# Optimization experiments

Hardware: AMD Instinct MI355X
Metric: run time of the kernel (lower is better)

## Reference

```python
import jax, jax.numpy as jnp
import numpy as np

V, D, H, L, F, S_MAX = 30522, 768, 12, 12, 3072, 512
B, S = 4, 512
HD = D // H
EPS = 1e-5

def setup_inputs():
    key = jax.random.key(0)
    ks = jax.random.split(key, 16)
    s = 0.02
    inp = {
        'input_ids': jax.random.randint(ks[0], (B, S), 0, V),
        'attention_mask': jnp.ones((B, S), dtype=jnp.int32),
        'word_emb': jax.random.normal(ks[1], (V, D)) * s,
        'pos_emb': jax.random.normal(ks[2], (S_MAX, D)) * s,
        'seg_emb': jax.random.normal(ks[3], (2, D)) * s,
        'emb_ln_g': jnp.ones((D,)), 'emb_ln_b': jnp.zeros((D,)),
        # per-layer stacked params, leading dim L
        'Wq': jax.random.normal(ks[4], (L, D, D)) * s,
        'Wk': jax.random.normal(ks[5], (L, D, D)) * s,
        'Wv': jax.random.normal(ks[6], (L, D, D)) * s,
        'Wo': jax.random.normal(ks[7], (L, D, D)) * s,
        'ff1_w': jax.random.normal(ks[8], (L, D, F)) * s,
        'ff1_b': jnp.zeros((L, F)),
        'ff2_w': jax.random.normal(ks[9], (L, F, D)) * s,
        'ff2_b': jnp.zeros((L, D)),
        'ln1_g': jnp.ones((L, D)), 'ln1_b': jnp.zeros((L, D)),
        'ln2_g': jnp.ones((L, D)), 'ln2_b': jnp.zeros((L, D)),
        'out_w': jax.random.normal(ks[10], (D, V)) * s,
        'out_b': jnp.zeros((V,)),
    }
    return inp

def _ln(x, g, b):
    mu = jnp.mean(x, axis=-1, keepdims=True)
    var = jnp.mean(jnp.square(x - mu), axis=-1, keepdims=True)
    return (x - mu) * jax.lax.rsqrt(var + EPS) * g + b

def reference(input_ids, attention_mask, word_emb, pos_emb, seg_emb,
              emb_ln_g, emb_ln_b, Wq, Wk, Wv, Wo, ff1_w, ff1_b, ff2_w, ff2_b,
              ln1_g, ln1_b, ln2_g, ln2_b, out_w, out_b):
    b, s = input_ids.shape
    # embeddings: word + position + segment (segment ids are all zero buffer)
    emb = word_emb[input_ids] + pos_emb[:s][None, :, :] + seg_emb[0][None, None, :]
    x = _ln(emb, emb_ln_g, emb_ln_b)  # [B,S,D]
    # key-position mask: True where masked out. [B,1,1,S]
    neg_mask = (attention_mask == 0)[:, None, None, :]
    scale = 1.0 / jnp.sqrt(jnp.asarray(D, x.dtype))  # NOTE: embed_dim, not head_dim

    def layer(x, p):
        wq, wk, wv, wo, f1w, f1b, f2w, f2b, g1, b1, g2, b2 = p
        q = (x @ wq).reshape(b, s, H, HD)
        k = (x @ wk).reshape(b, s, H, HD)
        v = (x @ wv).reshape(b, s, H, HD)
        scores = jnp.einsum('bqhd,bkhd->bhqk', q, k) * scale  # [B,H,S,S]
        scores = jnp.where(neg_mask, -jnp.inf, scores)
        attn = jax.nn.softmax(scores, axis=-1)
        o = jnp.einsum('bhqk,bkhd->bqhd', attn, v).reshape(b, s, D) @ wo
        x1 = _ln(x + o, g1, b1)
        h = jax.nn.gelu(x1 @ f1w + f1b, approximate=False)  # torch GELU is exact erf
        x2 = _ln(x1 + h @ f2w + f2b, g2, b2)
        return x2, attn

    x, attn_scores = jax.lax.scan(
        layer, x,
        (Wq, Wk, Wv, Wo, ff1_w, ff1_b, ff2_w, ff2_b, ln1_g, ln1_b, ln2_g, ln2_b))
    logits = x @ out_w + out_b  # [B,S,V]
    return logits, attn_scores  # attn_scores: [L,B,H,S,S]
```

## Files before the change

### kernel.cpp

```cpp
#include <hip/hip_runtime.h>
#include <hip/hip_bf16.h>

#define NLAYER 12
#define DMODEL 768
#define NHEAD  12
#define HDIM   64
#define FDIM   3072
#define VOCAB  30522
#define SLEN   512
#define NBATCH 4
#define NTOK   (NBATCH*SLEN)
#define EPSLN  1e-5f

typedef unsigned short u16;
using bf16 = __hip_bfloat16;
typedef __bf16 bf16x8 __attribute__((ext_vector_type(8)));
typedef float  f32x4  __attribute__((ext_vector_type(4)));
typedef u16    u16x4  __attribute__((ext_vector_type(4)));

__device__ __forceinline__ u16 f2bs(float f) {
    bf16 h = __float2bfloat16(f);
    return *reinterpret_cast<u16*>(&h);
}

__device__ __forceinline__ void gload_lds16(const void* g, void* l) {
    auto gp = (const __attribute__((address_space(1))) unsigned int*)g;
    auto lp = (__attribute__((address_space(3))) unsigned int*)(unsigned long long)l;
    __builtin_amdgcn_global_load_lds(gp, lp, 16, 0, 0);
}

template<int N> __device__ __forceinline__ void waitv() {
    if constexpr (N == 0)      asm volatile("s_waitcnt vmcnt(0)" ::: "memory");
    else if constexpr (N == 3) asm volatile("s_waitcnt vmcnt(3)" ::: "memory");
    else if constexpr (N == 4) asm volatile("s_waitcnt vmcnt(4)" ::: "memory");
    else if constexpr (N == 6) asm volatile("s_waitcnt vmcnt(6)" ::: "memory");
    else if constexpr (N == 8) asm volatile("s_waitcnt vmcnt(8)" ::: "memory");
}

__device__ __forceinline__ float wave_sum64(float v) {
#pragma unroll
    for (int off = 32; off > 0; off >>= 1) v += __shfl_down(v, off, 64);
    return v;
}
__device__ __forceinline__ float block_sum256(float v, float* red) {
    v = wave_sum64(v);
    __syncthreads();
    if ((threadIdx.x & 63) == 0) red[threadIdx.x >> 6] = v;
    __syncthreads();
    return red[0] + red[1] + red[2] + red[3];
}

__global__ __launch_bounds__(256) void embed_ln_kernel(
    const int* __restrict__ ids, const float* __restrict__ word,
    const float* __restrict__ pos, const float* __restrict__ seg,
    const float* __restrict__ g, const float* __restrict__ b,
    float* __restrict__ out, u16* __restrict__ outb)
{
    __shared__ float red[4];
    int t = blockIdx.x;
    int s = t & (SLEN - 1);
    long woff = (long)ids[t] * DMODEL;
    float vals[3];
#pragma unroll
    for (int i = 0; i < 3; i++) {
        int d = threadIdx.x + i * 256;
        vals[i] = word[woff + d] + pos[(long)s * DMODEL + d] + seg[d];
    }
    float mu = block_sum256(vals[0] + vals[1] + vals[2], red) * (1.0f / DMODEL);
    float vv = 0.f;
#pragma unroll
    for (int i = 0; i < 3; i++) { float d0 = vals[i] - mu; vv += d0 * d0; }
    float rstd = rsqrtf(block_sum256(vv, red) * (1.0f / DMODEL) + EPSLN);
#pragma unroll
    for (int i = 0; i < 3; i++) {
        int d = threadIdx.x + i * 256;
        float r = (vals[i] - mu) * rstd * g[d] + b[d];
        out[(long)t * DMODEL + d] = r;
        outb[(long)t * DMODEL + d] = f2bs(r);
    }
}

__global__ __launch_bounds__(256) void ln_res2_kernel(
    const float* __restrict__ a, const float* __restrict__ p0,
    const float* __restrict__ p1, const float* __restrict__ cbias,
    const float* __restrict__ g, const float* __restrict__ beta,
    float* __restrict__ out, u16* __restrict__ outb)
{
    __shared__ float red[4];
    long t = blockIdx.x;
    float vals[3];
#pragma unroll
    for (int i = 0; i < 3; i++) {
        int d = threadIdx.x + i * 256;
        float bb = cbias ? cbias[d] : 0.f;
        vals[i] = a[t * DMODEL + d] + p0[t * DMODEL + d] + p1[t * DMODEL + d] + bb;
    }
    float mu = block_sum256(vals[0] + vals[1] + vals[2], red) * (1.0f / DMODEL);
    float vv = 0.f;
#pragma unroll
    for (int i = 0; i < 3; i++) { float d0 = vals[i] - mu; vv += d0 * d0; }
    float rstd = rsqrtf(block_sum256(vv, red) * (1.0f / DMODEL) + EPSLN);
#pragma unroll
    for (int i = 0; i < 3; i++) {
        int d = threadIdx.x + i * 256;
        float r = (vals[i] - mu) * rstd * g[d] + beta[d];
        out[t * DMODEL + d] = r;
        outb[t * DMODEL + d] = f2bs(r);
    }
}

__global__ __launch_bounds__(256) void ln_res4_kernel(
    const float* __restrict__ a, const float* __restrict__ p0,
    const float* __restrict__ p1, const float* __restrict__ p2,
    const float* __restrict__ p3, const float* __restrict__ cbias,
    const float* __restrict__ g, const float* __restrict__ beta,
    float* __restrict__ out, u16* __restrict__ outb)
{
    __shared__ float red[4];
    long t = blockIdx.x;
    float vals[3];
#pragma unroll
    for (int i = 0; i < 3; i++) {
        int d = threadIdx.x + i * 256;
        vals[i] = a[t * DMODEL + d] + p0[t * DMODEL + d] + p1[t * DMODEL + d]
                + p2[t * DMODEL + d] + p3[t * DMODEL + d] + cbias[d];
    }
    float mu = block_sum256(vals[0] + vals[1] + vals[2], red) * (1.0f / DMODEL);
    float vv = 0.f;
#pragma unroll
    for (int i = 0; i < 3; i++) { float d0 = vals[i] - mu; vv += d0 * d0; }
    float rstd = rsqrtf(block_sum256(vv, red) * (1.0f / DMODEL) + EPSLN);
#pragma unroll
    for (int i = 0; i < 3; i++) {
        int d = threadIdx.x + i * 256;
        float r = (vals[i] - mu) * rstd * g[d] + beta[d];
        out[t * DMODEL + d] = r;
        outb[t * DMODEL + d] = f2bs(r);
    }
}

#define DD (DMODEL*DMODEL)
#define DF (DMODEL*FDIM)
#define LAYER_W_ELEMS (4*DD + 2*DF)
#define TILES_DD 576
#define TILES_DF 2304
#define TILES_LAYER (4*TILES_DD + 2*TILES_DF)
#define TILES_ALL (NLAYER*TILES_LAYER)
#define NTX_OW ((VOCAB + 31) / 32)
#define TILES_OW (NTX_OW * (DMODEL/32))

__global__ __launch_bounds__(256) void conv_all_kernel(
    const float* __restrict__ Wq, const float* __restrict__ Wk,
    const float* __restrict__ Wv, const float* __restrict__ Wo,
    const float* __restrict__ F1w, const float* __restrict__ F2w,
    const float* __restrict__ OutW, u16* __restrict__ wT, u16* __restrict__ owT)
{
    __shared__ float t[32][33];
    int id = blockIdx.x;
    const float* src; u16* dst; int K, N, tt;
    if (id < TILES_ALL) {
        int l = id / TILES_LAYER, r = id - l * TILES_LAYER;
        u16* base = wT + (long)l * LAYER_W_ELEMS;
        if (r < TILES_DD)           { src = Wq  + (long)l * DD; dst = base;            K = DMODEL; N = DMODEL; tt = r; }
        else if (r < 2 * TILES_DD)  { src = Wk  + (long)l * DD; dst = base + DD;       K = DMODEL; N = DMODEL; tt = r - TILES_DD; }
        else if (r < 3 * TILES_DD)  { src = Wv  + (long)l * DD; dst = base + 2 * DD;   K = DMODEL; N = DMODEL; tt = r - 2 * TILES_DD; }
        else if (r < 4 * TILES_DD)  { src = Wo  + (long)l * DD; dst = base + 3 * DD;   K = DMODEL; N = DMODEL; tt = r - 3 * TILES_DD; }
        else if (r < 4 * TILES_DD + TILES_DF)
                                    { src = F1w + (long)l * DF; dst = base + 4 * DD;   K = DMODEL; N = FDIM;   tt = r - 4 * TILES_DD; }
        else                        { src = F2w + (long)l * DF; dst = base + 4 * DD + DF; K = FDIM; N = DMODEL; tt = r - 4 * TILES_DD - TILES_DF; }
    } else {
        src = OutW; dst = owT; K = DMODEL; N = VOCAB; tt = id - TILES_ALL;
    }
    int ntx = (N + 31) >> 5;
    int n0 = (tt % ntx) * 32, k0 = (tt / ntx) * 32;
    int tx = threadIdx.x & 31, ty = threadIdx.x >> 5;
#pragma unroll
    for (int i = 0; i < 32; i += 8) {
        int k = k0 + ty + i, n = n0 + tx;
        t[ty + i][tx] = (k < K && n < N) ? src[(long)k * N + n] : 0.f;
    }
    __syncthreads();
#pragma unroll
    for (int i = 0; i < 32; i += 8) {
        int n = n0 + ty + i, k = k0 + tx;
        if (n < N && k < K) dst[(long)n * K + k] = f2bs(t[tx][ty + i]);
    }
}

__global__ __launch_bounds__(256, 2) void attn_kernel(
    const u16* __restrict__ qkvb, const u16* __restrict__ vtb,
    const int* __restrict__ amask,
    float* __restrict__ attn, u16* __restrict__ ob)
{
    __shared__ u16 Qs[64][64];
    __shared__ u16 Ks[SLEN][64];
    __shared__ float maskadd[SLEN];
    __shared__ __align__(16) float redA[64][4];
    __shared__ __align__(16) float redB[64][4];

    u16* Ph = &Ks[0][0];
    u16* Vh = &Ks[256][0];

    int z = blockIdx.y;
    int b = z / NHEAD, h = z - b * NHEAD;
    int m0 = blockIdx.x * 64;
    int tid = threadIdx.x;
    int wave = tid >> 6, lane = tid & 63;
    int quad = lane >> 4, l16 = lane & 15;
    const float scale = 0.036084391824351615f;

    for (int i = tid; i < SLEN; i += 256)
        maskadd[i] = amask[b * SLEN + i] ? 0.f : -1e30f;

    const u16* Qbase = qkvb + (long)(b * SLEN) * (3 * DMODEL) + h * HDIM;
    const u16* Kbase = Qbase + DMODEL;
    const u16* Vtbase = vtb + (long)z * HDIM * SLEN;

#pragma unroll
    for (int i = 0; i < 2; i++) {
        int off = wave * 2048 + i * 1024 + lane * 16;
        int row = off >> 7, c = (off >> 4) & 7, g = c ^ (row & 7);
        gload_lds16(Qbase + (long)(m0 + row) * (3 * DMODEL) + g * 8,
                    (char*)&Qs[0][0] + wave * 2048 + i * 1024);
    }
#pragma unroll
    for (int i = 0; i < 16; i++) {
        int off = wave * 16384 + i * 1024 + lane * 16;
        int row = off >> 7, c = (off >> 4) & 7, g = c ^ (row & 7);
        gload_lds16(Kbase + (long)row * (3 * DMODEL) + g * 8,
                    (char*)&Ks[0][0] + wave * 16384 + i * 1024);
    }
    __syncthreads();

    f32x4 acc[4][8];
#pragma unroll
    for (int i = 0; i < 4; i++)
#pragma unroll
        for (int j = 0; j < 8; j++) acc[i][j] = (f32x4){0.f, 0.f, 0.f, 0.f};

#pragma unroll
    for (int ks = 0; ks < 2; ks++) {
        bf16x8 afr[4], bfr[8];
#pragma unroll
        for (int i = 0; i < 4; i++) {
            int row = i * 16 + l16;
            int slot = ((ks << 2) + quad) ^ (row & 7);
            afr[i] = *reinterpret_cast<const bf16x8*>((char*)&Qs[0][0] + row * 128 + slot * 16);
        }
#pragma unroll
        for (int j = 0; j < 8; j++) {
            int row = wave * 128 + j * 16 + l16;
            int slot = ((ks << 2) + quad) ^ (row & 7);
            bfr[j] = *reinterpret_cast<const bf16x8*>((char*)&Ks[0][0] + row * 128 + slot * 16);
        }
#pragma unroll
        for (int i = 0; i < 4; i++)
#pragma unroll
            for (int j = 0; j < 8; j++)
                acc[i][j] = __builtin_amdgcn_mfma_f32_16x16x32_bf16(afr[i], bfr[j], acc[i][j], 0, 0, 0);
    }

    float ma[8];
#pragma unroll
    for (int j = 0; j < 8; j++) ma[j] = maskadd[wave * 128 + j * 16 + l16];

    float rmax[4][4];
#pragma unroll
    for (int i = 0; i < 4; i++)
#pragma unroll
        for (int r = 0; r < 4; r++) {
            float m = -3e38f;
#pragma unroll
            for (int j = 0; j < 8; j++) m = fmaxf(m, acc[i][j][r] * scale + ma[j]);
            rmax[i][r] = m;
        }
#pragma unroll
    for (int off = 1; off < 16; off <<= 1)
#pragma unroll
        for (int i = 0; i < 4; i++)
#pragma unroll
            for (int r = 0; r < 4; r++)
                rmax[i][r] = fmaxf(rmax[i][r], __shfl_xor(rmax[i][r], off, 64));
    if (l16 == 0) {
#pragma unroll
        for (int i = 0; i < 4; i++)
#pragma unroll
            for (int r = 0; r < 4; r++) redA[i * 16 + quad * 4 + r][wave] = rmax[i][r];
    }
    __syncthreads();

    {
        const u16* Vb = Vtbase + 0;
#pragma unroll
        for (int i = 0; i < 8; i++) {
            int o = wave * 8192 + i * 1024 + lane * 16;
            int hd = o >> 9, c = (o >> 4) & 31, g = c ^ (hd & 7);
            gload_lds16(Vb + (long)hd * SLEN + g * 8, (char*)Vh + wave * 8192 + i * 1024);
        }
    }

#pragma unroll
    for (int i = 0; i < 4; i++)
#pragma unroll
        for (int r = 0; r < 4; r++) {
            f32x4 v = *reinterpret_cast<const f32x4*>(&redA[i * 16 + quad * 4 + r][0]);
            rmax[i][r] = fmaxf(fmaxf(v[0], v[1]), fmaxf(v[2], v[3]));
        }

    float rsum[4][4];
#pragma unroll
    for (int i = 0; i < 4; i++)
#pragma unroll
        for (int r = 0; r < 4; r++) {
            float s = 0.f;
#pragma unroll
            for (int j = 0; j < 8; j++) {
                float e = expf(acc[i][j][r] * scale + ma[j] - rmax[i][r]);
                acc[i][j][r] = e;
                s += e;
            }
            rsum[i][r] = s;
        }
#pragma unroll
    for (int off = 1; off < 16; off <<= 1)
#pragma unroll
        for (int i = 0; i < 4; i++)
#pragma unroll
            for (int r = 0; r < 4; r++)
                rsum[i][r] += __shfl_xor(rsum[i][r], off, 64);
    if (l16 == 0) {
#pragma unroll
        for (int i = 0; i < 4; i++)
#pragma unroll
            for (int r = 0; r < 4; r++) redB[i * 16 + quad * 4 + r][wave] = rsum[i][r];
    }
    __syncthreads();

    float* ap = attn + (long)z * SLEN * SLEN;
#pragma unroll
    for (int i = 0; i < 4; i++)
#pragma unroll
        for (int r = 0; r < 4; r++) {
            f32x4 v = *reinterpret_cast<const f32x4*>(&redB[i * 16 + quad * 4 + r][0]);
            float inv = 1.0f / (v[0] + v[1] + v[2] + v[3]);
            long row = m0 + i * 16 + quad * 4 + r;
#pragma unroll
            for (int j = 0; j < 8; j++) {
                int col = (wave << 7) + j * 16 + l16;
                float p = acc[i][j][r] * inv;
                acc[i][j][r] = p;
                ap[row * SLEN + col] = p;
            }
        }

    if (wave < 2) {
#pragma unroll
        for (int i = 0; i < 4; i++)
#pragma unroll
            for (int j = 0; j < 8; j++) {
                int cl = (wave << 7) + j * 16 + l16;
#pragma unroll
                for (int r = 0; r < 4; r++) {
                    int row = i * 16 + quad * 4 + r;
                    int slot = (cl >> 3) ^ (row & 7);
                    *(u16*)((char*)Ph + row * 512 + slot * 16 + (cl & 7) * 2) = f2bs(acc[i][j][r]);
                }
            }
    }
    __syncthreads();

    f32x4 acc2[4];
#pragma unroll
    for (int j = 0; j < 4; j++) acc2[j] = (f32x4){0.f, 0.f, 0.f, 0.f};

#pragma unroll
    for (int step = 0; step < 8; step++) {
        int Prow = (wave << 4) + l16;
        int aslot = (step * 4 + quad) ^ (Prow & 7);
        bf16x8 af = *reinterpret_cast<const bf16x8*>((char*)Ph + Prow * 512 + aslot * 16);
#pragma unroll
        for (int j = 0; j < 4; j++) {
            int hd = j * 16 + l16;
            int bslot = (step * 4 + quad) ^ (hd & 7);
            bf16x8 bf = *reinterpret_cast<const bf16x8*>((char*)Vh + hd * 512 + bslot * 16);
            acc2[j] = __builtin_amdgcn_mfma_f32_16x16x32_bf16(af, bf, acc2[j], 0, 0, 0);
        }
    }
    __syncthreads();

    {
        const u16* Vb = Vtbase + 256;
#pragma unroll
        for (int i = 0; i < 8; i++) {
            int o = wave * 8192 + i * 1024 + lane * 16;
            int hd = o >> 9, c = (o >> 4) & 31, g = c ^ (hd & 7);
            gload_lds16(Vb + (long)hd * SLEN + g * 8, (char*)Vh + wave * 8192 + i * 1024);
        }
    }
    if (wave >= 2) {
#pragma unroll
        for (int i = 0; i < 4; i++)
#pragma unroll
            for (int j = 0; j < 8; j++) {
                int cl = ((wave - 2) << 7) + j * 16 + l16;
#pragma unroll
                for (int r = 0; r < 4; r++) {
                    int row = i * 16 + quad * 4 + r;
                    int slot = (cl >> 3) ^ (row & 7);
                    *(u16*)((char*)Ph + row * 512 + slot * 16 + (cl & 7) * 2) = f2bs(acc[i][j][r]);
                }
            }
    }
    __syncthreads();

#pragma unroll
    for (int step = 0; step < 8; step++) {
        int Prow = (wave << 4) + l16;
        int aslot = (step * 4 + quad) ^ (Prow & 7);
        bf16x8 af = *reinterpret_cast<const bf16x8*>((char*)Ph + Prow * 512 + aslot * 16);
#pragma unroll
        for (int j = 0; j < 4; j++) {
            int hd = j * 16 + l16;
            int bslot = (step * 4 + quad) ^ (hd & 7);
            bf16x8 bf = *reinterpret_cast<const bf16x8*>((char*)Vh + hd * 512 + bslot * 16);
            acc2[j] = __builtin_amdgcn_mfma_f32_16x16x32_bf16(af, bf, acc2[j], 0, 0, 0);
        }
    }

#pragma unroll
    for (int j = 0; j < 4; j++)
#pragma unroll
        for (int r = 0; r < 4; r++) {
            int q = m0 + (wave << 4) + quad * 4 + r;
            ob[((long)(b * SLEN + q)) * DMODEL + h * HDIM + j * 16 + l16] = f2bs(acc2[j][r]);
        }
}

template<int BM, int BN, int OUTBF, int GELU, int QKVF>
__global__ __launch_bounds__(256) void gemm_bf16(
    const u16* __restrict__ A, int lda, long sA1, long sA2,
    const u16* __restrict__ B, int ldb, long sB1, long sB2,
    void* __restrict__ Cv, int ldc, long sC1, long sC2,
    int zdiv, const float* __restrict__ bias,
    int N, int K, float scale, u16* __restrict__ vt)
{
    __shared__ u16 As[3][BM][32];
    __shared__ u16 Bs[3][BN][32];
    int z = blockIdx.z;
    int zq = z / zdiv, zr = z - zq * zdiv;
    A += zq * sA1 + zr * sA2;
    B += zq * sB1 + zr * sB2;

    int m0 = blockIdx.y * BM;
    int n0 = blockIdx.x * BN;
    int tid = threadIdx.x;
    int wave = tid >> 6, lane = tid & 63;
    int quad = lane >> 4, l16 = lane & 15;
    int wr = wave >> 1, wc = wave & 1;
    constexpr int MR = BM / 32, NR = BN / 32;
    constexpr int LPT = BM / 64 + BN / 64;

    f32x4 acc[MR][NR];
#pragma unroll
    for (int i = 0; i < MR; i++)
#pragma unroll
        for (int j = 0; j < NR; j++) acc[i][j] = (f32x4){0.f, 0.f, 0.f, 0.f};

    int srow = lane >> 2;
    int sc   = lane & 3;

    auto stage = [&](int buf, int k0) {
#pragma unroll
        for (int i = 0; i < BM / 64; i++) {
            int chunk = wave * (BM / 64) + i;
            int lrow = chunk * 16 + srow;
            int gcol = (sc ^ ((lrow >> 1) & 3)) * 8;
            gload_lds16(A + (long)(m0 + lrow) * lda + k0 + gcol, &As[buf][chunk * 16][0]);
        }
#pragma unroll
        for (int i = 0; i < BN / 64; i++) {
            int chunk = wave * (BN / 64) + i;
            int lrow = chunk * 16 + srow;
            int grow = n0 + lrow;
            if (grow > N - 1) grow = N - 1;
            int gcol = (sc ^ ((lrow >> 1) & 3)) * 8;
            gload_lds16(B + (long)grow * ldb + k0 + gcol, &Bs[buf][chunk * 16][0]);
        }
    };

    int nt = K >> 5;
    stage(0, 0);
    if (nt > 1) stage(1, 32);
    if (nt > 2) stage(2, 64);

    int cur = 0;
    for (int t = 0; t < nt; ++t) {
        if (t + 2 < nt)      waitv<2 * LPT>();
        else if (t + 1 < nt) waitv<LPT>();
        else                 waitv<0>();
        __builtin_amdgcn_s_barrier();
        __builtin_amdgcn_sched_barrier(0);

        bf16x8 afr[MR], bfr[NR];
#pragma unroll
        for (int i = 0; i < MR; i++) {
            int row = wr * (BM / 2) + i * 16 + l16;
            int slot = quad ^ ((row >> 1) & 3);
            afr[i] = *reinterpret_cast<const bf16x8*>((char*)&As[cur][0][0] + row * 64 + slot * 16);
        }
#pragma unroll
        for (int j = 0; j < NR; j++) {
            int row = wc * (BN / 2) + j * 16 + l16;
            int slot = quad ^ ((row >> 1) & 3);
            bfr[j] = *reinterpret_cast<const bf16x8*>((char*)&Bs[cur][0][0] + row * 64 + slot * 16);
        }
        __builtin_amdgcn_s_setprio(1);
#pragma unroll
        for (int i = 0; i < MR; i++)
#pragma unroll
            for (int j = 0; j < NR; j++)
                acc[i][j] = __builtin_amdgcn_mfma_f32_16x16x32_bf16(afr[i], bfr[j], acc[i][j], 0, 0, 0);
        __builtin_amdgcn_s_setprio(0);

        asm volatile("" ::: "memory");
        __builtin_amdgcn_sched_barrier(0);
        __builtin_amdgcn_s_barrier();
        __builtin_amdgcn_sched_barrier(0);
        if (t + 3 < nt) stage(cur, (t + 3) * 32);
        cur = cur + 1; if (cur == 3) cur = 0;
    }

    float* Cf = (float*)Cv;
    u16*   Cb = (u16*)Cv;
    long coff = zq * sC1 + zr * sC2;
#pragma unroll
    for (int i = 0; i < MR; i++) {
        int rbase = m0 + wr * (BM / 2) + i * 16 + quad * 4;
#pragma unroll
        for (int j = 0; j < NR; j++) {
            int col = n0 + wc * (BN / 2) + j * 16 + l16;
            if (col < N) {
                float badd = bias ? bias[col] : 0.f;
                u16x4 v4;
#pragma unroll
                for (int r = 0; r < 4; r++) {
                    float vv = acc[i][j][r] * scale + badd;
                    if (GELU) vv = 0.5f * vv * (1.0f + erff(vv * 0.70710678118f));
                    long idx = coff + (long)(rbase + r) * ldc + col;
                    if (OUTBF) { u16 u = f2bs(vv); Cb[idx] = u; v4[r] = u; }
                    else       Cf[idx] = vv;
                }
                if (QKVF && col >= 2 * DMODEL) {
                    int hh = (col - 2 * DMODEL) >> 6, hd = col & 63;
                    int bb = rbase >> 9, s = rbase & (SLEN - 1);
                    *reinterpret_cast<u16x4*>(
                        vt + ((long)(bb * NHEAD + hh) * HDIM + hd) * SLEN + s) = v4;
                }
            }
        }
    }
}

template<int BM, int BN, int OUTBF, int GELU, int QKVF = 0>
static inline void launch_gemm(hipStream_t stream,
    const u16* A, int lda, long sA1, long sA2,
    const u16* B, int ldb, long sB1, long sB2,
    void* C, int ldc, long sC1, long sC2,
    int zdiv, const float* bias, int M, int N, int K, float scale, int Z,
    u16* vt = nullptr)
{
    dim3 grid((N + BN - 1) / BN, M / BM, Z);
    gemm_bf16<BM, BN, OUTBF, GELU, QKVF><<<grid, 256, 0, stream>>>(
        A, lda, sA1, sA2, B, ldb, sB1, sB2, C, ldc, sC1, sC2,
        zdiv, bias, N, K, scale, vt);
}

extern "C" void kernel_launch(void* const* d_in, const int* in_sizes, int n_in,
                              void* d_out, int out_size, void* d_ws, size_t ws_size,
                              hipStream_t stream)
{
    const int*   ids   = (const int*)d_in[0];
    const int*   amask = (const int*)d_in[1];
    const float* word  = (const float*)d_in[2];
    const float* pos   = (const float*)d_in[3];
    const float* seg   = (const float*)d_in[4];
    const float* eg    = (const float*)d_in[5];
    const float* eb    = (const float*)d_in[6];
    const float* Wq    = (const float*)d_in[7];
    const float* Wk    = (const float*)d_in[8];
    const float* Wv    = (const float*)d_in[9];
    const float* Wo    = (const float*)d_in[10];
    const float* F1w   = (const float*)d_in[11];
    const float* F1b   = (const float*)d_in[12];
    const float* F2w   = (const float*)d_in[13];
    const float* F2b   = (const float*)d_in[14];
    const float* G1    = (const float*)d_in[15];
    const float* B1    = (const float*)d_in[16];
    const float* G2    = (const float*)d_in[17];
    const float* B2    = (const float*)d_in[18];
    const float* OutW  = (const float*)d_in[19];
    const float* OutB  = (const float*)d_in[20];

    float* logits = (float*)d_out;
    float* attn_base = logits + (long)NTOK * VOCAB;

    long nd = (long)NTOK * DMODEL;
    float* x  = (float*)d_ws;
    float* x1 = x + nd;
    float* p0 = x1 + nd;
    float* p1 = p0 + nd;
    float* p2 = p1 + nd;
    float* p3 = p2 + nd;
    u16* xb   = (u16*)(p3 + nd);
    u16* x1b  = xb + nd;
    u16* qkvb = x1b + nd;
    u16* vtb  = qkvb + (long)NTOK * 3 * DMODEL;
    u16* ob   = vtb + nd;
    u16* hb   = ob + nd;
    u16* wT   = hb + (long)NTOK * FDIM;
    u16* owT  = wT + (long)NLAYER * LAYER_W_ELEMS;

    conv_all_kernel<<<TILES_ALL + TILES_OW, 256, 0, stream>>>(
        Wq, Wk, Wv, Wo, F1w, F2w, OutW, wT, owT);

    embed_ln_kernel<<<NTOK, 256, 0, stream>>>(ids, word, pos, seg, eg, eb, x, xb);

    for (int l = 0; l < NLAYER; l++) {
        const u16* qkvT = wT + (long)l * LAYER_W_ELEMS;
        const u16* woT  = qkvT + 3 * DD;
        const u16* f1T  = qkvT + 4 * DD;
        const u16* f2T  = qkvT + 4 * DD + DF;
        const float* f1b = F1b + (long)l * FDIM;
        const float* f2b = F2b + (long)l * DMODEL;
        float* attn_l = attn_base + (long)l * NBATCH * NHEAD * SLEN * SLEN;

        launch_gemm<128, 128, 1, 0, 1>(stream, xb, DMODEL, 0, 0,
                                       qkvT, DMODEL, 0, 0,
                                       qkvb, 3 * DMODEL, 0, 0,
                                       1, nullptr, NTOK, 3 * DMODEL, DMODEL, 1.f, 1, vtb);

        attn_kernel<<<dim3(SLEN / 64, NBATCH * NHEAD), 256, 0, stream>>>(
            qkvb, vtb, amask, attn_l, ob);

        launch_gemm<128, 64, 0, 0>(stream, ob, DMODEL, 384, 0,
                                   woT, DMODEL, 384, 0,
                                   p0, DMODEL, nd, 0,
                                   1, nullptr, NTOK, DMODEL, 384, 1.f, 2);

        ln_res2_kernel<<<NTOK, 256, 0, stream>>>(x, p0, p1, nullptr,
                                                 G1 + (long)l * DMODEL, B1 + (long)l * DMODEL, x1, x1b);

        launch_gemm<128, 128, 1, 1>(stream, x1b, DMODEL, 0, 0,
                                    f1T, DMODEL, 0, 0,
                                    hb, FDIM, 0, 0,
                                    1, f1b, NTOK, FDIM, DMODEL, 1.f, 1);

        launch_gemm<128, 128, 0, 0>(stream, hb, FDIM, 768, 0,
                                    f2T, FDIM, 768, 0,
                                    p0, DMODEL, nd, 0,
                                    1, nullptr, NTOK, DMODEL, 768, 1.f, 4);

        ln_res4_kernel<<<NTOK, 256, 0, stream>>>(x1, p0, p1, p2, p3, f2b,
                                                 G2 + (long)l * DMODEL, B2 + (long)l * DMODEL, x, xb);
    }

    launch_gemm<128, 128, 0, 0>(stream, xb, DMODEL, 0, 0,
                                owT, DMODEL, 0, 0,
                                logits, VOCAB, 0, 0,
                                1, OutB, NTOK, VOCAB, DMODEL, 1.f, 1);
}
```

Before: 1.907 ms.

## Restructure GEMM to 512 threads, K-tile 64 with double buffering

The bf16 GEMM moves from 256 to 512 threads per block, laid out as a 2x4 wave grid, so each wave now covers half as many N columns. The K tile grows from 32 to 64 with a new XOR swizzle over 8 slots, and the pipeline drops from triple to double buffering. The aim is fewer barriers per unit of K and more waves to hide latency. In exchange each wave does less work per barrier and keeps only one prefetch stage in flight, and the stage code assumes BM and BN are multiples of 64.

Result: faster. 1.758 ms (-7.8%).

```diff
diff --git a/kernel.cpp b/kernel.cpp
--- a/kernel.cpp
+++ b/kernel.cpp
@@ -437,15 +437,15 @@
 }
 
 template<int BM, int BN, int OUTBF, int GELU, int QKVF>
-__global__ __launch_bounds__(256) void gemm_bf16(
+__global__ __launch_bounds__(512) void gemm_bf16(
     const u16* __restrict__ A, int lda, long sA1, long sA2,
     const u16* __restrict__ B, int ldb, long sB1, long sB2,
     void* __restrict__ Cv, int ldc, long sC1, long sC2,
     int zdiv, const float* __restrict__ bias,
     int N, int K, float scale, u16* __restrict__ vt)
 {
-    __shared__ u16 As[3][BM][32];
-    __shared__ u16 Bs[3][BN][32];
+    __shared__ u16 As[2][BM][64];
+    __shared__ u16 Bs[2][BN][64];
     int z = blockIdx.z;
     int zq = z / zdiv, zr = z - zq * zdiv;
     A += zq * sA1 + zr * sA2;
@@ -456,9 +456,10 @@
     int tid = threadIdx.x;
     int wave = tid >> 6, lane = tid & 63;
     int quad = lane >> 4, l16 = lane & 15;
-    int wr = wave >> 1, wc = wave & 1;
-    constexpr int MR = BM / 32, NR = BN / 32;
-    constexpr int LPT = BM / 64 + BN / 64;
+    int wr = wave >> 2, wc = wave & 3;
+    constexpr int MR = BM / 32, NR = BN / 64;
+    constexpr int PA = BM / 64, PB = BN / 64;
+    constexpr int LPT = PA + PB;
 
     f32x4 acc[MR][NR];
 #pragma unroll
@@ -466,68 +467,69 @@
 #pragma unroll
         for (int j = 0; j < NR; j++) acc[i][j] = (f32x4){0.f, 0.f, 0.f, 0.f};
 
-    int srow = lane >> 2;
-    int sc   = lane & 3;
-
     auto stage = [&](int buf, int k0) {
 #pragma unroll
-        for (int i = 0; i < BM / 64; i++) {
-            int chunk = wave * (BM / 64) + i;
-            int lrow = chunk * 16 + srow;
-            int gcol = (sc ^ ((lrow >> 1) & 3)) * 8;
-            gload_lds16(A + (long)(m0 + lrow) * lda + k0 + gcol, &As[buf][chunk * 16][0]);
-        }
-#pragma unroll
-        for (int i = 0; i < BN / 64; i++) {
-            int chunk = wave * (BN / 64) + i;
-            int lrow = chunk * 16 + srow;
-            int grow = n0 + lrow;
+        for (int p = 0; p < PA; p++) {
+            int chunk = p * 512 + tid;
+            int row = chunk >> 3, sc = chunk & 7;
+            int gcol = (sc ^ (row & 7)) * 8;
+            gload_lds16(A + (long)(m0 + row) * lda + k0 + gcol,
+                        (char*)&As[buf][0][0] + p * 8192 + wave * 1024);
+        }
+#pragma unroll
+        for (int p = 0; p < PB; p++) {
+            int chunk = p * 512 + tid;
+            int row = chunk >> 3, sc = chunk & 7;
+            int grow = n0 + row;
             if (grow > N - 1) grow = N - 1;
-            int gcol = (sc ^ ((lrow >> 1) & 3)) * 8;
-            gload_lds16(B + (long)grow * ldb + k0 + gcol, &Bs[buf][chunk * 16][0]);
+            int gcol = (sc ^ (row & 7)) * 8;
+            gload_lds16(B + (long)grow * ldb + k0 + gcol,
+                        (char*)&Bs[buf][0][0] + p * 8192 + wave * 1024);
         }
     };
 
-    int nt = K >> 5;
+    int nt = K >> 6;
     stage(0, 0);
-    if (nt > 1) stage(1, 32);
-    if (nt > 2) stage(2, 64);
-
-    int cur = 0;
+    if (nt > 1) stage(1, 64);
+
     for (int t = 0; t < nt; ++t) {
-        if (t + 2 < nt)      waitv<2 * LPT>();
-        else if (t + 1 < nt) waitv<LPT>();
-        else                 waitv<0>();
+        if (t + 1 < nt) waitv<LPT>();
+        else            waitv<0>();
         __builtin_amdgcn_s_barrier();
         __builtin_amdgcn_sched_barrier(0);
 
-        bf16x8 afr[MR], bfr[NR];
-#pragma unroll
-        for (int i = 0; i < MR; i++) {
-            int row = wr * (BM / 2) + i * 16 + l16;
-            int slot = quad ^ ((row >> 1) & 3);
-            afr[i] = *reinterpret_cast<const bf16x8*>((char*)&As[cur][0][0] + row * 64 + slot * 16);
-        }
-#pragma unroll
-        for (int j = 0; j < NR; j++) {
-            int row = wc * (BN / 2) + j * 16 + l16;
-            int slot = quad ^ ((row >> 1) & 3);
-            bfr[j] = *reinterpret_cast<const bf16x8*>((char*)&Bs[cur][0][0] + row * 64 + slot * 16);
-        }
-        __builtin_amdgcn_s_setprio(1);
-#pragma unroll
-        for (int i = 0; i < MR; i++)
-#pragma unroll
-            for (int j = 0; j < NR; j++)
-                acc[i][j] = __builtin_amdgcn_mfma_f32_16x16x32_bf16(afr[i], bfr[j], acc[i][j], 0, 0, 0);
-        __builtin_amdgcn_s_setprio(0);
+        int cur = t & 1;
+#pragma unroll
+        for (int kh = 0; kh < 2; kh++) {
+            bf16x8 afr[MR], bfr[NR];
+#pragma unroll
+            for (int i = 0; i < MR; i++) {
+                int row = wr * (BM / 2) + i * 16 + l16;
+                int slot = ((kh << 2) + quad) ^ (row & 7);
+                afr[i] = *reinterpret_cast<const bf16x8*>(
+                    (char*)&As[cur][0][0] + row * 128 + slot * 16);
+            }
+#pragma unroll
+            for (int j = 0; j < NR; j++) {
+                int row = wc * (BN / 4) + j * 16 + l16;
+                int slot = ((kh << 2) + quad) ^ (row & 7);
+                bfr[j] = *reinterpret_cast<const bf16x8*>(
+                    (char*)&Bs[cur][0][0] + row * 128 + slot * 16);
+            }
+            __builtin_amdgcn_s_setprio(1);
+#pragma unroll
+            for (int i = 0; i < MR; i++)
+#pragma unroll
+                for (int j = 0; j < NR; j++)
+                    acc[i][j] = __builtin_amdgcn_mfma_f32_16x16x32_bf16(afr[i], bfr[j], acc[i][j], 0, 0, 0);
+            __builtin_amdgcn_s_setprio(0);
+        }
 
         asm volatile("" ::: "memory");
         __builtin_amdgcn_sched_barrier(0);
         __builtin_amdgcn_s_barrier();
         __builtin_amdgcn_sched_barrier(0);
-        if (t + 3 < nt) stage(cur, (t + 3) * 32);
-        cur = cur + 1; if (cur == 3) cur = 0;
+        if (t + 2 < nt) stage(cur, (t + 2) << 6);
     }
 
     float* Cf = (float*)Cv;
@@ -538,7 +540,7 @@
         int rbase = m0 + wr * (BM / 2) + i * 16 + quad * 4;
 #pragma unroll
         for (int j = 0; j < NR; j++) {
-            int col = n0 + wc * (BN / 2) + j * 16 + l16;
+            int col = n0 + wc * (BN / 4) + j * 16 + l16;
             if (col < N) {
                 float badd = bias ? bias[col] : 0.f;
                 u16x4 v4;
@@ -570,7 +572,7 @@
     u16* vt = nullptr)
 {
     dim3 grid((N + BN - 1) / BN, M / BM, Z);
-    gemm_bf16<BM, BN, OUTBF, GELU, QKVF><<<grid, 256, 0, stream>>>(
+    gemm_bf16<BM, BN, OUTBF, GELU, QKVF><<<grid, 512, 0, stream>>>(
         A, lda, sA1, sA2, B, ldb, sB1, sB2, C, ldc, sC1, sC2,
         zdiv, bias, N, K, scale, vt);
 }
```
